# Kernel optimization log

Measured on AMD Instinct MI355X. Metric: run time of the kernel, lower is better.

Reference implementation:

```python
import jax, jax.numpy as jnp
import numpy as np

ROPE_BASE = 10000.0
NEG = -1e9

def _rope_tables(N, head_dim, dtype):
    # freq buffer: angles[pos, i] = pos / base^(2i/head_dim), i over half dim
    inv = 1.0 / (ROPE_BASE ** (jnp.arange(0, head_dim, 2, dtype=jnp.float32) / head_dim))
    ang = jnp.arange(N, dtype=jnp.float32)[:, None] * inv[None, :]  # (N, hd/2)
    return jnp.cos(ang).astype(dtype), jnp.sin(ang).astype(dtype)

def _apply_rope(t, cos, sin):
    # t: (B, h, N, hd); rotate-half style
    hd = t.shape[-1]
    t1, t2 = t[..., : hd // 2], t[..., hd // 2 :]
    c = cos[None, None]  # (1,1,N,hd/2)
    s = sin[None, None]
    return jnp.concatenate([t1 * c - t2 * s, t1 * s + t2 * c], axis=-1)


def setup_inputs() -> dict:
    key = jax.random.key(0)
    B, N, D, h = 2, 2048, 2048, 16
    ks = jax.random.split(key, 5)
    x = jax.random.normal(ks[0], (B, N, D), dtype=jnp.float32)
    Wqkv = jax.random.normal(ks[1], (3 * D, D), dtype=jnp.float32) * 0.02
    Wproj = jax.random.normal(ks[2], (D, D), dtype=jnp.float32) * 0.02
    bproj = jax.random.normal(ks[3], (D,), dtype=jnp.float32) * 0.02
    L = jax.random.randint(ks[4], (B,), 1, N + 1, dtype=jnp.int32)
    return {"x": x, "Wqkv": Wqkv, "Wproj": Wproj, "bproj": bproj, "L": L, "n_heads": 16}


def reference(x, Wqkv, Wproj, bproj, L, n_heads):
    B, N, D = x.shape
    hd = D // n_heads
    scale = 1.0 / jnp.sqrt(jnp.asarray(hd, dtype=x.dtype))

    # fused QKV projection (no bias)
    qkv = jnp.einsum('bnd,ed->bne', x, Wqkv)  # (B, N, 3D)
    q, k, v = jnp.split(qkv, 3, axis=-1)
    # (B, N, h*hd) -> (B, h, N, hd)
    def heads(t):
        return t.reshape(B, N, n_heads, hd).transpose(0, 2, 1, 3)
    q, k, v = heads(q), heads(k), heads(v)

    cos, sin = _rope_tables(N, hd, x.dtype)
    q = _apply_rope(q, cos, sin)
    k = _apply_rope(k, cos, sin)

    # causal + key-padding mask (pos < L valid)
    pos = jnp.arange(N)
    causal = pos[:, None] >= pos[None, :]                    # (N, N)
    key_valid = pos[None, :] < L[:, None]                    # (B, N)
    mask = causal[None, None] & key_valid[:, None, None, :]  # (B,1,N,N)

    scores = jnp.einsum('bhqd,bhkd->bhqk', q, k) * scale
    scores = jnp.where(mask, scores, NEG)
    attn = jax.nn.softmax(scores, axis=-1)
    out = jnp.einsum('bhqk,bhkd->bhqd', attn, v)             # (B,h,N,hd)
    out = out.transpose(0, 2, 1, 3).reshape(B, N, D)
    return jnp.einsum('bnd,ed->bne', out, Wproj) + bproj
```

## Files before the change

### kernel.cpp

```cpp
#include <hip/hip_runtime.h>
#include <hip/hip_bf16.h>


typedef unsigned short u16;
typedef short bf16x8 __attribute__((ext_vector_type(8)));
typedef unsigned short u16x8 __attribute__((ext_vector_type(8)));
typedef float f32x4 __attribute__((ext_vector_type(4)));

#define MFMA16(a, b, c) __builtin_amdgcn_mfma_f32_16x16x32_bf16((a), (b), (c), 0, 0, 0)

__device__ __forceinline__ float b2f(u16 u) { return __uint_as_float(((unsigned)u) << 16); }
__device__ __forceinline__ u16 f2b(float f) {
    unsigned x = __float_as_uint(f);
    return (u16)((x + 0x7fffu + ((x >> 16) & 1u)) >> 16);
}
__device__ __forceinline__ void gload16(const u16* g, u16* lds) {
    __builtin_amdgcn_global_load_lds((__attribute__((address_space(1))) void*)g,
                                     (__attribute__((address_space(3))) void*)lds,
                                     16, 0, 0);
}

__global__ __launch_bounds__(256) void cvt_bf16(const float* __restrict__ in,
                                                u16* __restrict__ out) {
    size_t i = (size_t)blockIdx.x * 256 + threadIdx.x;
    float4 a = ((const float4*)in)[2 * i];
    float4 b = ((const float4*)in)[2 * i + 1];
    u16x8 o;
    o[0] = f2b(a.x); o[1] = f2b(a.y); o[2] = f2b(a.z); o[3] = f2b(a.w);
    o[4] = f2b(b.x); o[5] = f2b(b.y); o[6] = f2b(b.z); o[7] = f2b(b.w);
    ((u16x8*)out)[i] = o;
}

__global__ __launch_bounds__(256) void rope_tables_k(float* __restrict__ cosT,
                                                     float* __restrict__ sinT) {
    int idx = blockIdx.x * 256 + threadIdx.x;
    int n = idx >> 6, i = idx & 63;
    float inv = powf(10000.0f, -(float)(2 * i) / 128.0f);
    float ang = (float)n * inv;
    cosT[idx] = cosf(ang);
    sinT[idx] = sinf(ang);
}

template <int OUTF32>
__global__ __launch_bounds__(256, 2) void gemm_nt(const u16* __restrict__ A,
                                                  const u16* __restrict__ B,
                                                  void* __restrict__ Cv,
                                                  const float* __restrict__ bias,
                                                  int Ncols, int K, int lgnbx) {
    __shared__ u16 As[128 * 64];
    __shared__ u16 Bs[128 * 64];
    const int tx = threadIdx.x;
    const int w = tx >> 6, l = tx & 63;
    const int fr = l & 15, fg = l >> 4;
    const int wr = w >> 1, wc = w & 1;
    int id = blockIdx.x;
    const int cpx = (int)gridDim.x >> 3;
    id = (id & 7) * cpx + (id >> 3);
    const long row0 = (long)(id & ((1 << lgnbx) - 1)) * 128;
    const long col0 = (long)(id >> lgnbx) * 128;
    f32x4 acc[4][4] = {};
    const int nk = K >> 6;
    int rs[4], ss[4];
#pragma unroll
    for (int i = 0; i < 4; ++i) {
        int c = i * 256 + tx;
        rs[i] = c >> 3;
        ss[i] = (c & 7) ^ ((c >> 3) & 7);
    }
    for (int kt = 0; kt < nk; ++kt) {
        const long k0 = (long)kt << 6;
        __syncthreads();
#pragma unroll
        for (int i = 0; i < 4; ++i)
            gload16(A + (row0 + rs[i]) * K + k0 + ss[i] * 8, &As[(i * 256 + w * 64) * 8]);
#pragma unroll
        for (int i = 0; i < 4; ++i)
            gload16(B + (col0 + rs[i]) * K + k0 + ss[i] * 8, &Bs[(i * 256 + w * 64) * 8]);
        __syncthreads();
#pragma unroll
        for (int kk = 0; kk < 2; ++kk) {
            bf16x8 af[4], bfv[4];
#pragma unroll
            for (int m = 0; m < 4; ++m) {
                int r = wr * 64 + m * 16 + fr;
                af[m] = *(const bf16x8*)&As[r * 64 + (((kk * 4 + fg) ^ (r & 7)) << 3)];
            }
#pragma unroll
            for (int n = 0; n < 4; ++n) {
                int r = wc * 64 + n * 16 + fr;
                bfv[n] = *(const bf16x8*)&Bs[r * 64 + (((kk * 4 + fg) ^ (r & 7)) << 3)];
            }
#pragma unroll
            for (int m = 0; m < 4; ++m)
#pragma unroll
                for (int n = 0; n < 4; ++n) acc[m][n] = MFMA16(af[m], bfv[n], acc[m][n]);
        }
    }
#pragma unroll
    for (int m = 0; m < 4; ++m) {
#pragma unroll
        for (int n = 0; n < 4; ++n) {
#pragma unroll
            for (int r = 0; r < 4; ++r) {
                long row = row0 + wr * 64 + m * 16 + fg * 4 + r;
                long col = col0 + wc * 64 + n * 16 + fr;
                float v = acc[m][n][r];
                if (OUTF32) {
                    ((float*)Cv)[row * Ncols + col] = v + bias[col];
                } else {
                    ((u16*)Cv)[row * Ncols + col] = f2b(v);
                }
            }
        }
    }
}

__global__ __launch_bounds__(256) void rope_transpose_k(
    const u16* __restrict__ qkv, const float* __restrict__ cosT,
    const float* __restrict__ sinT, u16* __restrict__ Q, u16* __restrict__ Ko,
    u16* __restrict__ VT) {
    const int bh = blockIdx.y, b = bh >> 4, h = bh & 15;
    const int n0 = blockIdx.x << 7;
    const int tx = threadIdx.x;
    __shared__ u16 vbuf[128][136];
    const float SCALE = 0.08838834764831844f;
#pragma unroll
    for (int pass = 0; pass < 4; ++pass) {
        const int rr = pass * 32 + (tx >> 3);
        const int p = tx & 7;
        const int n = n0 + rr;
        const u16* src = qkv + ((size_t)(b * 2048 + n)) * 6144 + h * 128;
        float c[8], s[8];
#pragma unroll
        for (int j = 0; j < 8; ++j) {
            c[j] = cosT[n * 64 + p * 8 + j];
            s[j] = sinT[n * 64 + p * 8 + j];
        }
        {
            u16x8 t1 = *(const u16x8*)&src[p * 8];
            u16x8 t2 = *(const u16x8*)&src[64 + p * 8];
            u16x8 o1, o2;
#pragma unroll
            for (int j = 0; j < 8; ++j) {
                float a = b2f(t1[j]), bb = b2f(t2[j]);
                o1[j] = f2b((a * c[j] - bb * s[j]) * SCALE);
                o2[j] = f2b((a * s[j] + bb * c[j]) * SCALE);
            }
            u16* dst = Q + ((size_t)bh * 2048 + n) * 128;
            *(u16x8*)&dst[p * 8] = o1;
            *(u16x8*)&dst[64 + p * 8] = o2;
        }
        {
            u16x8 t1 = *(const u16x8*)&src[2048 + p * 8];
            u16x8 t2 = *(const u16x8*)&src[2048 + 64 + p * 8];
            u16x8 o1, o2;
#pragma unroll
            for (int j = 0; j < 8; ++j) {
                float a = b2f(t1[j]), bb = b2f(t2[j]);
                o1[j] = f2b(a * c[j] - bb * s[j]);
                o2[j] = f2b(a * s[j] + bb * c[j]);
            }
            u16* dst = Ko + ((size_t)bh * 2048 + n) * 128;
            *(u16x8*)&dst[p * 8] = o1;
            *(u16x8*)&dst[64 + p * 8] = o2;
        }
    }
#pragma unroll
    for (int i = 0; i < 8; ++i) {
        int cid = i * 256 + tx;
        int rr = cid >> 4, cc = cid & 15;
        *(u16x8*)&vbuf[rr][cc * 8] =
            *(const u16x8*)&qkv[((size_t)(b * 2048 + n0 + rr)) * 6144 + 4096 + h * 128 + cc * 8];
    }
    __syncthreads();
#pragma unroll
    for (int i = 0; i < 8; ++i) {
        int cid = i * 256 + tx;
        int j = cid >> 4, nc = cid & 15;
        u16x8 o;
#pragma unroll
        for (int e = 0; e < 8; ++e) o[e] = vbuf[nc * 8 + e][j];
        *(u16x8*)&VT[((size_t)bh * 128 + j) * 2048 + n0 + nc * 8] = o;
    }
}

__global__ __launch_bounds__(256, 2) void attn_k(const u16* __restrict__ Q,
                                                 const u16* __restrict__ K,
                                                 const u16* __restrict__ VT,
                                                 u16* __restrict__ O,
                                                 const int* __restrict__ L) {
    const int bh = blockIdx.y, b = bh >> 4, h = bh & 15;
    const int qx = blockIdx.x;
    const int qb0 = qx << 6, qb1 = (31 - qx) << 6;
    const int tx = threadIdx.x;
    const int w = tx >> 6, l = tx & 63;
    const int fr = l & 15, fg = l >> 4;
    const int Lb = L[b];
    __shared__ u16 Ks[2][64 * 128];
    __shared__ u16 Vs[2][128 * 64];
    __shared__ u16 Ps[4][16 * 72];
    const u16* Qh = Q + (size_t)bh * 2048 * 128;
    const u16* Kh = K + (size_t)bh * 2048 * 128;
    const u16* Vh = VT + (size_t)bh * 128 * 2048;
    bf16x8 aq0[4], aq1[4];
#pragma unroll
    for (int kc = 0; kc < 4; ++kc) {
        aq0[kc] = *(const bf16x8*)&Qh[(size_t)(qb0 + w * 16 + fr) * 128 + kc * 32 + fg * 8];
        aq1[kc] = *(const bf16x8*)&Qh[(size_t)(qb1 + w * 16 + fr) * 128 + kc * 32 + fg * 8];
    }
    f32x4 accO0[8] = {}, accO1[8] = {};
    float mr0[4] = {-1e30f, -1e30f, -1e30f, -1e30f};
    float mr1[4] = {-1e30f, -1e30f, -1e30f, -1e30f};
    float sr0[4] = {0.f, 0.f, 0.f, 0.f};
    float sr1[4] = {0.f, 0.f, 0.f, 0.f};
    const int kmax = min(qb1 + 63, Lb - 1);
    const int nkt = (kmax >> 6) + 1;

    auto stage_tile = [&](int kt0, int buf) {
#pragma unroll
        for (int i = 0; i < 4; ++i) {
            int c = i * 256 + tx;
            int row = c >> 4, cp = c & 15;
            gload16(Kh + (size_t)(kt0 + row) * 128 + ((cp ^ (row & 7)) << 3),
                    &Ks[buf][(i * 256 + w * 64) * 8]);
        }
#pragma unroll
        for (int i = 0; i < 4; ++i) {
            int c = i * 256 + tx;
            int row = c >> 3, cp = c & 7;
            gload16(Vh + (size_t)row * 2048 + kt0 + ((cp ^ (row & 7)) << 3),
                    &Vs[buf][(i * 256 + w * 64) * 8]);
        }
    };

    auto do_strip = [&](const bf16x8 (&aqs)[4], float (&mr)[4], float (&sr)[4],
                        f32x4 (&aO)[8], int qgb, int kt0, const u16* Ksb,
                        const u16* Vsb) {
        f32x4 accS[4];
#pragma unroll
        for (int st = 0; st < 4; ++st) {
            f32x4 z = {0.f, 0.f, 0.f, 0.f};
            accS[st] = z;
            int key = st * 16 + fr;
#pragma unroll
            for (int kc = 0; kc < 4; ++kc) {
                bf16x8 bk = *(const bf16x8*)&Ksb[key * 128 + (((kc * 4 + fg) ^ (key & 7)) << 3)];
                accS[st] = MFMA16(aqs[kc], bk, accS[st]);
            }
        }
        float sv[4][4];
        if ((kt0 + 63 <= qgb) && (kt0 + 63 < Lb)) {
#pragma unroll
            for (int st = 0; st < 4; ++st)
#pragma unroll
                for (int r = 0; r < 4; ++r) sv[st][r] = accS[st][r];
        } else {
#pragma unroll
            for (int st = 0; st < 4; ++st)
#pragma unroll
                for (int r = 0; r < 4; ++r) {
                    int key = kt0 + st * 16 + fr;
                    int qg = qgb + fg * 4 + r;
                    sv[st][r] = (key <= qg && key < Lb) ? accS[st][r] : -1e30f;
                }
        }
        float alpha[4], pr[4][4];
#pragma unroll
        for (int r = 0; r < 4; ++r) {
            float lm = fmaxf(fmaxf(sv[0][r], sv[1][r]), fmaxf(sv[2][r], sv[3][r]));
            lm = fmaxf(lm, __shfl_xor(lm, 1));
            lm = fmaxf(lm, __shfl_xor(lm, 2));
            lm = fmaxf(lm, __shfl_xor(lm, 4));
            lm = fmaxf(lm, __shfl_xor(lm, 8));
            float mn = fmaxf(mr[r], lm);
            alpha[r] = exp2f((mr[r] - mn) * 1.44269504f);
            float ls = 0.f;
#pragma unroll
            for (int st = 0; st < 4; ++st) {
                float p = exp2f((sv[st][r] - mn) * 1.44269504f);
                pr[st][r] = p;
                ls += p;
            }
            ls += __shfl_xor(ls, 1);
            ls += __shfl_xor(ls, 2);
            ls += __shfl_xor(ls, 4);
            ls += __shfl_xor(ls, 8);
            sr[r] = sr[r] * alpha[r] + ls;
            mr[r] = mn;
        }
#pragma unroll
        for (int n = 0; n < 8; ++n)
#pragma unroll
            for (int r = 0; r < 4; ++r) aO[n][r] *= alpha[r];
#pragma unroll
        for (int st = 0; st < 4; ++st)
#pragma unroll
            for (int r = 0; r < 4; ++r)
                Ps[w][(fg * 4 + r) * 72 + st * 16 + fr] = f2b(pr[st][r]);
#pragma unroll
        for (int ks = 0; ks < 2; ++ks) {
            bf16x8 ap = *(const bf16x8*)&Ps[w][fr * 72 + ks * 32 + fg * 8];
#pragma unroll
            for (int n = 0; n < 8; ++n) {
                int d = n * 16 + fr;
                bf16x8 bv = *(const bf16x8*)&Vsb[d * 64 + (((ks * 4 + fg) ^ (d & 7)) << 3)];
                aO[n] = MFMA16(ap, bv, aO[n]);
            }
        }
    };

    stage_tile(0, 0);
    int cur = 0;
    for (int kt = 0; kt < nkt; ++kt) {
        const int kt0 = kt << 6;
        __syncthreads();
        if (kt + 1 < nkt) stage_tile((kt + 1) << 6, cur ^ 1);
        if (kt <= qx)
            do_strip(aq0, mr0, sr0, accO0, qb0 + w * 16, kt0, Ks[cur], Vs[cur]);
        do_strip(aq1, mr1, sr1, accO1, qb1 + w * 16, kt0, Ks[cur], Vs[cur]);
        cur ^= 1;
    }
    float inv0[4], inv1[4];
#pragma unroll
    for (int r = 0; r < 4; ++r) {
        inv0[r] = 1.0f / sr0[r];
        inv1[r] = 1.0f / sr1[r];
    }
#pragma unroll
    for (int n = 0; n < 8; ++n)
#pragma unroll
        for (int r = 0; r < 4; ++r) {
            int d = n * 16 + fr;
            int q0 = qb0 + w * 16 + fg * 4 + r;
            int q1 = qb1 + w * 16 + fg * 4 + r;
            O[((size_t)(b * 2048 + q0)) * 2048 + h * 128 + d] = f2b(accO0[n][r] * inv0[r]);
            O[((size_t)(b * 2048 + q1)) * 2048 + h * 128 + d] = f2b(accO1[n][r] * inv1[r]);
        }
}

extern "C" void kernel_launch(void* const* d_in, const int* in_sizes, int n_in,
                              void* d_out, int out_size, void* d_ws, size_t ws_size,
                              hipStream_t stream) {
    const float* x = (const float*)d_in[0];
    const float* Wqkv = (const float*)d_in[1];
    const float* Wproj = (const float*)d_in[2];
    const float* bproj = (const float*)d_in[3];
    const int* L = (const int*)d_in[4];
    float* out = (float*)d_out;

    char* p = (char*)d_ws;
    u16* xbf = (u16*)(p + 0);
    u16* wqkvbf = (u16*)(p + 16777216);
    u16* wprojbf = (u16*)(p + 41943040);
    u16* qkv = (u16*)(p + 50331648);
    u16* Kb = (u16*)(p + 100663296);
    u16* VTb = (u16*)(p + 117440512);
    float* cosT = (float*)(p + 134217728);
    float* sinT = (float*)(p + 134742016);
    u16* Ob = xbf;
    u16* Qb = wqkvbf;

    cvt_bf16<<<4096, 256, 0, stream>>>(x, xbf);
    cvt_bf16<<<6144, 256, 0, stream>>>(Wqkv, wqkvbf);
    cvt_bf16<<<2048, 256, 0, stream>>>(Wproj, wprojbf);
    rope_tables_k<<<512, 256, 0, stream>>>(cosT, sinT);
    gemm_nt<0><<<1536, 256, 0, stream>>>(xbf, wqkvbf, qkv, nullptr, 6144, 2048, 5);
    rope_transpose_k<<<dim3(16, 32), 256, 0, stream>>>(qkv, cosT, sinT, Qb, Kb, VTb);
    attn_k<<<dim3(16, 32), 256, 0, stream>>>(Qb, Kb, VTb, Ob, L);
    gemm_nt<1><<<512, 256, 0, stream>>>(Ob, wprojbf, out, bproj, 2048, 2048, 5);
}
```

Measured before the change: 277.8 us.

## Replace QKV GEMM with 256x256 multi-stage pipelined kernel and fuse conversions

The QKV projection GEMM is rewritten as a 512-thread kernel with 256x256 tiles. It uses double-buffered LDS split into half-K slices, interleaves global-to-LDS loads with MFMA quads, and sets explicit waitcnt, barriers and s_setprio. The aim is to hide memory latency and raise MFMA utilisation in the largest GEMM. The three fp32-to-bf16 conversion launches are merged into one kernel to cut launch overhead. The output GEMM moves to a separate non-templated kernel with a plain grid mapping, so it loses the previous block-swizzle.

```diff
diff --git a/kernel.cpp b/kernel.cpp
--- a/kernel.cpp
+++ b/kernel.cpp
@@ -8,6 +8,11 @@
 typedef float f32x4 __attribute__((ext_vector_type(4)));
 
 #define MFMA16(a, b, c) __builtin_amdgcn_mfma_f32_16x16x32_bf16((a), (b), (c), 0, 0, 0)
+#define BAR() asm volatile("s_barrier" ::: "memory")
+#define WAITV(N) asm volatile("s_waitcnt vmcnt(" #N ")" ::: "memory")
+#define WAITL0()                                       \
+    asm volatile("s_waitcnt lgkmcnt(0)" ::: "memory"); \
+    __builtin_amdgcn_sched_barrier(0)
 
 __device__ __forceinline__ float b2f(u16 u) { return __uint_as_float(((unsigned)u) << 16); }
 __device__ __forceinline__ u16 f2b(float f) {
@@ -20,15 +25,29 @@
                                      16, 0, 0);
 }
 
-__global__ __launch_bounds__(256) void cvt_bf16(const float* __restrict__ in,
-                                                u16* __restrict__ out) {
-    size_t i = (size_t)blockIdx.x * 256 + threadIdx.x;
-    float4 a = ((const float4*)in)[2 * i];
-    float4 b = ((const float4*)in)[2 * i + 1];
+__global__ __launch_bounds__(256) void cvt3(const float* __restrict__ x,
+                                            const float* __restrict__ wqkv,
+                                            const float* __restrict__ wproj,
+                                            u16* __restrict__ xo, u16* __restrict__ qo,
+                                            u16* __restrict__ po) {
+    const int bx = blockIdx.x;
+    const float* src;
+    u16* dst;
+    size_t base;
+    if (bx < 4096) {
+        src = x; dst = xo; base = (size_t)bx * 256;
+    } else if (bx < 10240) {
+        src = wqkv; dst = qo; base = (size_t)(bx - 4096) * 256;
+    } else {
+        src = wproj; dst = po; base = (size_t)(bx - 10240) * 256;
+    }
+    size_t i = base + threadIdx.x;
+    float4 a = ((const float4*)src)[2 * i];
+    float4 b = ((const float4*)src)[2 * i + 1];
     u16x8 o;
     o[0] = f2b(a.x); o[1] = f2b(a.y); o[2] = f2b(a.z); o[3] = f2b(a.w);
     o[4] = f2b(b.x); o[5] = f2b(b.y); o[6] = f2b(b.z); o[7] = f2b(b.w);
-    ((u16x8*)out)[i] = o;
+    ((u16x8*)dst)[i] = o;
 }
 
 __global__ __launch_bounds__(256) void rope_tables_k(float* __restrict__ cosT,
@@ -41,78 +60,133 @@
     sinT[idx] = sinf(ang);
 }
 
-template <int OUTF32>
-__global__ __launch_bounds__(256, 2) void gemm_nt(const u16* __restrict__ A,
-                                                  const u16* __restrict__ B,
-                                                  void* __restrict__ Cv,
-                                                  const float* __restrict__ bias,
-                                                  int Ncols, int K, int lgnbx) {
-    __shared__ u16 As[128 * 64];
-    __shared__ u16 Bs[128 * 64];
+template <int MB>
+__device__ __forceinline__ void quad(f32x4 (&acc)[8][4], const bf16x8 (&af)[4],
+                                     const bf16x8 (&bf)[4]) {
+#pragma unroll
+    for (int j = 0; j < 4; ++j)
+#pragma unroll
+        for (int n = 0; n < 4; ++n)
+            acc[MB * 4 + j][n] = MFMA16(af[j], bf[n], acc[MB * 4 + j][n]);
+}
+
+__global__ __launch_bounds__(512, 1) void gemm8_nt(const u16* __restrict__ A,
+                                                   const u16* __restrict__ B,
+                                                   u16* __restrict__ C,
+                                                   int M, int Nc, int K, int ntn) {
+    __shared__ __align__(16) u16 AS[2][2][256 * 32];
+    __shared__ __align__(16) u16 BS[2][2][256 * 32];
     const int tx = threadIdx.x;
     const int w = tx >> 6, l = tx & 63;
     const int fr = l & 15, fg = l >> 4;
-    const int wr = w >> 1, wc = w & 1;
-    int id = blockIdx.x;
-    const int cpx = (int)gridDim.x >> 3;
-    id = (id & 7) * cpx + (id >> 3);
-    const long row0 = (long)(id & ((1 << lgnbx) - 1)) * 128;
-    const long col0 = (long)(id >> lgnbx) * 128;
-    f32x4 acc[4][4] = {};
-    const int nk = K >> 6;
-    int rs[4], ss[4];
-#pragma unroll
-    for (int i = 0; i < 4; ++i) {
-        int c = i * 256 + tx;
-        rs[i] = c >> 3;
-        ss[i] = (c & 7) ^ ((c >> 3) & 7);
-    }
-    for (int kt = 0; kt < nk; ++kt) {
-        const long k0 = (long)kt << 6;
-        __syncthreads();
-#pragma unroll
-        for (int i = 0; i < 4; ++i)
-            gload16(A + (row0 + rs[i]) * K + k0 + ss[i] * 8, &As[(i * 256 + w * 64) * 8]);
-#pragma unroll
-        for (int i = 0; i < 4; ++i)
-            gload16(B + (col0 + rs[i]) * K + k0 + ss[i] * 8, &Bs[(i * 256 + w * 64) * 8]);
-        __syncthreads();
-#pragma unroll
-        for (int kk = 0; kk < 2; ++kk) {
-            bf16x8 af[4], bfv[4];
-#pragma unroll
-            for (int m = 0; m < 4; ++m) {
-                int r = wr * 64 + m * 16 + fr;
-                af[m] = *(const bf16x8*)&As[r * 64 + (((kk * 4 + fg) ^ (r & 7)) << 3)];
-            }
-#pragma unroll
-            for (int n = 0; n < 4; ++n) {
-                int r = wc * 64 + n * 16 + fr;
-                bfv[n] = *(const bf16x8*)&Bs[r * 64 + (((kk * 4 + fg) ^ (r & 7)) << 3)];
-            }
-#pragma unroll
-            for (int m = 0; m < 4; ++m)
-#pragma unroll
-                for (int n = 0; n < 4; ++n) acc[m][n] = MFMA16(af[m], bfv[n], acc[m][n]);
-        }
-    }
-#pragma unroll
-    for (int m = 0; m < 4; ++m) {
-#pragma unroll
-        for (int n = 0; n < 4; ++n) {
-#pragma unroll
-            for (int r = 0; r < 4; ++r) {
-                long row = row0 + wr * 64 + m * 16 + fg * 4 + r;
-                long col = col0 + wc * 64 + n * 16 + fr;
-                float v = acc[m][n][r];
-                if (OUTF32) {
-                    ((float*)Cv)[row * Ncols + col] = v + bias[col];
-                } else {
-                    ((u16*)Cv)[row * Ncols + col] = f2b(v);
-                }
-            }
-        }
-    }
+    const int wr = w >> 2, wc = w & 3;
+    const int id = blockIdx.x;
+    const int tm = id / ntn, tn = id % ntn;
+    const size_t row0 = (size_t)tm * 256, col0 = (size_t)tn * 256;
+    const u16* Ab = A + row0 * (size_t)K;
+    const u16* Bb = B + col0 * (size_t)K;
+    const int nt = K >> 6, tmask = nt - 1;
+
+    const int r0c = tx >> 2, s0 = (tx & 3) ^ ((r0c >> 1) & 3);
+    const int r1c = (512 + tx) >> 2, s1 = ((512 + tx) & 3) ^ ((r1c >> 1) & 3);
+    const int d0 = (w * 64) * 8, d1 = (512 + w * 64) * 8;
+    auto stage = [&](const u16* src, u16* reg) {
+        gload16(src + (size_t)r0c * K + s0 * 8, reg + d0);
+        gload16(src + (size_t)r1c * K + s1 * 8, reg + d1);
+    };
+    auto frag = [&](const u16* reg, int r) {
+        return *(const bf16x8*)&reg[r * 32 + ((fg ^ ((r >> 1) & 3)) << 3)];
+    };
+
+    f32x4 acc[8][4] = {};
+    const int a0 = wr * 128, b0c = wc * 64;
+
+    stage(Bb + 0, BS[0][0]);
+    stage(Ab + 0, AS[0][0]);
+    stage(Bb + 32, BS[0][1]);
+    stage(Ab + 32, AS[0][1]);
+    stage(Bb + 64, BS[1][0]);
+    stage(Ab + 64, AS[1][0]);
+    stage(Bb + 64 + 32, BS[1][1]);
+    WAITV(6);
+    BAR();
+
+    bf16x8 afrag[4], bfrag[4];
+    for (int i = 0; i < (nt >> 1); ++i) {
+        const int t = 2 * i;
+        const size_t o1 = (size_t)((t + 1) & tmask) * 64;
+        const size_t o2 = (size_t)((t + 2) & tmask) * 64;
+        const size_t o3 = (size_t)((t + 3) & tmask) * 64;
+#pragma unroll
+        for (int j = 0; j < 4; ++j) afrag[j] = frag(AS[0][0], a0 + j * 16 + fr);
+#pragma unroll
+        for (int n = 0; n < 4; ++n) bfrag[n] = frag(BS[0][0], b0c + n * 16 + fr);
+        stage(Ab + o1 + 32, AS[1][1]);
+        BAR(); WAITL0();
+        __builtin_amdgcn_s_setprio(1); quad<0>(acc, afrag, bfrag); __builtin_amdgcn_s_setprio(0);
+        BAR();
+#pragma unroll
+        for (int j = 0; j < 4; ++j) afrag[j] = frag(AS[0][0], a0 + 64 + j * 16 + fr);
+        stage(Bb + o2, BS[0][0]);
+        BAR(); WAITL0();
+        __builtin_amdgcn_s_setprio(1); quad<1>(acc, afrag, bfrag); __builtin_amdgcn_s_setprio(0);
+        BAR();
+#pragma unroll
+        for (int j = 0; j < 4; ++j) afrag[j] = frag(AS[0][1], a0 + j * 16 + fr);
+#pragma unroll
+        for (int n = 0; n < 4; ++n) bfrag[n] = frag(BS[0][1], b0c + n * 16 + fr);
+        stage(Ab + o2, AS[0][0]);
+        BAR(); WAITL0();
+        __builtin_amdgcn_s_setprio(1); quad<0>(acc, afrag, bfrag); __builtin_amdgcn_s_setprio(0);
+        BAR();
+#pragma unroll
+        for (int j = 0; j < 4; ++j) afrag[j] = frag(AS[0][1], a0 + 64 + j * 16 + fr);
+        stage(Bb + o2 + 32, BS[0][1]);
+        WAITV(6);
+        BAR(); WAITL0();
+        __builtin_amdgcn_s_setprio(1); quad<1>(acc, afrag, bfrag); __builtin_amdgcn_s_setprio(0);
+        BAR();
+#pragma unroll
+        for (int j = 0; j < 4; ++j) afrag[j] = frag(AS[1][0], a0 + j * 16 + fr);
+#pragma unroll
+        for (int n = 0; n < 4; ++n) bfrag[n] = frag(BS[1][0], b0c + n * 16 + fr);
+        stage(Ab + o2 + 32, AS[0][1]);
+        BAR(); WAITL0();
+        __builtin_amdgcn_s_setprio(1); quad<0>(acc, afrag, bfrag); __builtin_amdgcn_s_setprio(0);
+        BAR();
+#pragma unroll
+        for (int j = 0; j < 4; ++j) afrag[j] = frag(AS[1][0], a0 + 64 + j * 16 + fr);
+        stage(Bb + o3, BS[1][0]);
+        BAR(); WAITL0();
+        __builtin_amdgcn_s_setprio(1); quad<1>(acc, afrag, bfrag); __builtin_amdgcn_s_setprio(0);
+        BAR();
+#pragma unroll
+        for (int j = 0; j < 4; ++j) afrag[j] = frag(AS[1][1], a0 + j * 16 + fr);
+#pragma unroll
+        for (int n = 0; n < 4; ++n) bfrag[n] = frag(BS[1][1], b0c + n * 16 + fr);
+        stage(Ab + o3, AS[1][0]);
+        BAR(); WAITL0();
+        __builtin_amdgcn_s_setprio(1); quad<0>(acc, afrag, bfrag); __builtin_amdgcn_s_setprio(0);
+        BAR();
+#pragma unroll
+        for (int j = 0; j < 4; ++j) afrag[j] = frag(AS[1][1], a0 + 64 + j * 16 + fr);
+        stage(Bb + o3 + 32, BS[1][1]);
+        WAITV(6);
+        BAR(); WAITL0();
+        __builtin_amdgcn_s_setprio(1); quad<1>(acc, afrag, bfrag); __builtin_amdgcn_s_setprio(0);
+        BAR();
+    }
+    asm volatile("s_waitcnt vmcnt(0)" ::: "memory");
+#pragma unroll
+    for (int m = 0; m < 8; ++m)
+#pragma unroll
+        for (int n = 0; n < 4; ++n)
+#pragma unroll
+            for (int rr = 0; rr < 4; ++rr) {
+                size_t row = row0 + a0 + m * 16 + fg * 4 + rr;
+                size_t col = col0 + b0c + n * 16 + fr;
+                C[row * (size_t)Nc + col] = f2b(acc[m][n][rr]);
+            }
 }
 
 __global__ __launch_bounds__(256) void rope_transpose_k(
@@ -182,6 +256,69 @@
         for (int e = 0; e < 8; ++e) o[e] = vbuf[nc * 8 + e][j];
         *(u16x8*)&VT[((size_t)bh * 128 + j) * 2048 + n0 + nc * 8] = o;
     }
+}
+
+__global__ __launch_bounds__(256, 2) void gemm_nt_f32(const u16* __restrict__ A,
+                                                      const u16* __restrict__ B,
+                                                      float* __restrict__ C,
+                                                      const float* __restrict__ bias,
+                                                      int Ncols, int K) {
+    __shared__ u16 As[128 * 64];
+    __shared__ u16 Bs[128 * 64];
+    const int tx = threadIdx.x;
+    const int w = tx >> 6, l = tx & 63;
+    const int fr = l & 15, fg = l >> 4;
+    const int wr = w >> 1, wc = w & 1;
+    const long row0 = (long)blockIdx.x * 128;
+    const long col0 = (long)blockIdx.y * 128;
+    f32x4 acc[4][4] = {};
+    const int nk = K >> 6;
+    int rs[4], ss[4];
+#pragma unroll
+    for (int i = 0; i < 4; ++i) {
+        int c = i * 256 + tx;
+        rs[i] = c >> 3;
+        ss[i] = (c & 7) ^ ((c >> 3) & 7);
+    }
+    for (int kt = 0; kt < nk; ++kt) {
+        const long k0 = (long)kt << 6;
+        __syncthreads();
+#pragma unroll
+        for (int i = 0; i < 4; ++i)
+            gload16(A + (row0 + rs[i]) * K + k0 + ss[i] * 8, &As[(i * 256 + w * 64) * 8]);
+#pragma unroll
+        for (int i = 0; i < 4; ++i)
+            gload16(B + (col0 + rs[i]) * K + k0 + ss[i] * 8, &Bs[(i * 256 + w * 64) * 8]);
+        __syncthreads();
+#pragma unroll
+        for (int kk = 0; kk < 2; ++kk) {
+            bf16x8 af[4], bfv[4];
+#pragma unroll
+            for (int m = 0; m < 4; ++m) {
+                int r = wr * 64 + m * 16 + fr;
+                af[m] = *(const bf16x8*)&As[r * 64 + (((kk * 4 + fg) ^ (r & 7)) << 3)];
+            }
+#pragma unroll
+            for (int n = 0; n < 4; ++n) {
+                int r = wc * 64 + n * 16 + fr;
+                bfv[n] = *(const bf16x8*)&Bs[r * 64 + (((kk * 4 + fg) ^ (r & 7)) << 3)];
+            }
+#pragma unroll
+            for (int m = 0; m < 4; ++m)
+#pragma unroll
+                for (int n = 0; n < 4; ++n) acc[m][n] = MFMA16(af[m], bfv[n], acc[m][n]);
+        }
+    }
+#pragma unroll
+    for (int m = 0; m < 4; ++m)
+#pragma unroll
+        for (int n = 0; n < 4; ++n)
+#pragma unroll
+            for (int r = 0; r < 4; ++r) {
+                long row = row0 + wr * 64 + m * 16 + fg * 4 + r;
+                long col = col0 + wc * 64 + n * 16 + fr;
+                C[row * Ncols + col] = acc[m][n][r] + bias[col];
+            }
 }
 
 __global__ __launch_bounds__(256, 2) void attn_k(const u16* __restrict__ Q,
@@ -360,12 +497,10 @@
     u16* Ob = xbf;
     u16* Qb = wqkvbf;
 
-    cvt_bf16<<<4096, 256, 0, stream>>>(x, xbf);
-    cvt_bf16<<<6144, 256, 0, stream>>>(Wqkv, wqkvbf);
-    cvt_bf16<<<2048, 256, 0, stream>>>(Wproj, wprojbf);
+    cvt3<<<12288, 256, 0, stream>>>(x, Wqkv, Wproj, xbf, wqkvbf, wprojbf);
     rope_tables_k<<<512, 256, 0, stream>>>(cosT, sinT);
-    gemm_nt<0><<<1536, 256, 0, stream>>>(xbf, wqkvbf, qkv, nullptr, 6144, 2048, 5);
+    gemm8_nt<<<384, 512, 0, stream>>>(xbf, wqkvbf, qkv, 4096, 6144, 2048, 24);
     rope_transpose_k<<<dim3(16, 32), 256, 0, stream>>>(qkv, cosT, sinT, Qb, Kb, VTb);
     attn_k<<<dim3(16, 32), 256, 0, stream>>>(Qb, Kb, VTb, Ob, L);
-    gemm_nt<1><<<512, 256, 0, stream>>>(Ob, wprojbf, out, bproj, 2048, 2048, 5);
-}
+    gemm_nt_f32<<<dim3(32, 16), 256, 0, stream>>>(Ob, wprojbf, out, bproj, 2048, 2048);
+}
```

Result: no change. 280.2 us (+0.9%).
